# Kernel optimization log

Hardware: AMD Instinct MI355X
Metric: run time of the kernel (lower is better)

The kernel has to match this reference:

```python
import jax, jax.numpy as jnp
import numpy as np

WS = (7, 7, 7)  # window size (h, w, d)
N = WS[0] * WS[1] * WS[2]  # 343
DIM = 192
H = 6
B = 512
NW = 64  # number of distinct window masks; B % NW == 0


def _make_rel_table():
    ch = np.arange(-(WS[0] - 1), WS[0], dtype=np.float32)
    cw = np.arange(-(WS[1] - 1), WS[1], dtype=np.float32)
    cd = np.arange(-(WS[2] - 1), WS[2], dtype=np.float32)
    tbl = np.stack(np.meshgrid(ch, cw, cd, indexing='ij'), axis=-1)[None]  # [1,13,13,13,3]
    tbl[..., 0] /= WS[0] - 1
    tbl[..., 1] /= WS[1] - 1
    tbl[..., 2] /= WS[2] - 1
    tbl *= 8
    tbl = np.sign(tbl) * np.log2(np.abs(tbl) + 1.0) / np.log2(8)
    return tbl.astype(np.float32)


def _make_rp_index():
    coords = np.stack(np.meshgrid(np.arange(WS[0]), np.arange(WS[1]), np.arange(WS[2]), indexing='ij'))
    cf = coords.reshape(3, -1)  # [3, N]
    rel = cf[:, :, None] - cf[:, None, :]  # [3, N, N]
    rel = rel.transpose(1, 2, 0).copy()
    rel[..., 0] += WS[0] - 1
    rel[..., 1] += WS[1] - 1
    rel[..., 2] += WS[2] - 1
    rel[..., 0] *= (2 * WS[1] - 1) * (2 * WS[2] - 1)
    rel[..., 1] *= 2 * WS[2] - 1
    return rel.sum(-1).astype(np.int32)  # [N, N]


def setup_inputs() -> dict:
    key = jax.random.key(0)
    ks = jax.random.split(key, 10)
    s = 0.02
    return {
        'x': jax.random.normal(ks[0], (B, N, DIM), jnp.float32),
        'y': jax.random.normal(ks[1], (B, N, DIM), jnp.float32),
        'mask': jnp.where(jax.random.uniform(ks[2], (NW, N, N)) > 0.5, 0.0, -100.0).astype(jnp.float32),
        'qkv1_w': jax.random.normal(ks[3], (3 * DIM, DIM), jnp.float32) * s,
        'qkv2_w': jax.random.normal(ks[4], (3 * DIM, DIM), jnp.float32) * s,
        'q1_bias': jnp.zeros((DIM,), jnp.float32),
        'v1_bias': jnp.zeros((DIM,), jnp.float32),
        'q2_bias': jnp.zeros((DIM,), jnp.float32),
        'v2_bias': jnp.zeros((DIM,), jnp.float32),
        'logit_scale': jnp.log(10.0 * jnp.ones((H, 1, 1), jnp.float32)),
        'cpb_w1': jax.random.normal(ks[5], (512, 3), jnp.float32) * s,
        'cpb_b1': jnp.zeros((512,), jnp.float32),
        'cpb_w2': jax.random.normal(ks[6], (H, 512), jnp.float32) * s,
        'proj_w': jax.random.normal(ks[7], (DIM, DIM), jnp.float32) * s,
        'proj_b': jnp.zeros((DIM,), jnp.float32),
        'rel_table': jnp.asarray(_make_rel_table()),
        'rp_index': jnp.asarray(_make_rp_index()),
    }


def reference(x, y, mask, qkv1_w, qkv2_w, q1_bias, v1_bias, q2_bias, v2_bias,
              logit_scale, cpb_w1, cpb_b1, cpb_w2, proj_w, proj_b, rel_table, rp_index):
    B_, N_, C = x.shape
    hd = C // H
    qkv1_b = jnp.concatenate([q1_bias, jnp.zeros_like(v1_bias), v1_bias])
    qkv2_b = jnp.concatenate([q2_bias, jnp.zeros_like(v2_bias), v2_bias])
    # [B, N, 3C] -> [3, B, H, N, hd]
    qkv1 = (x @ qkv1_w.T + qkv1_b).reshape(B_, N_, 3, H, hd).transpose(2, 0, 3, 1, 4)
    qkv2 = (y @ qkv2_w.T + qkv2_b).reshape(B_, N_, 3, H, hd).transpose(2, 0, 3, 1, 4)
    q, k, v = qkv2[0], qkv1[1], qkv1[2]
    # cosine attention
    qn = q / jnp.linalg.norm(q, axis=-1, keepdims=True).clip(1e-12)
    kn = k / jnp.linalg.norm(k, axis=-1, keepdims=True).clip(1e-12)
    attn = jnp.einsum('bhnd,bhmd->bhnm', qn, kn)
    scale = jnp.exp(jnp.minimum(logit_scale, jnp.log(jnp.float32(100.0))))
    attn = attn * scale[None]  # [B,H,N,N]
    # continuous position bias
    hbias = jax.nn.relu(rel_table @ cpb_w1.T + cpb_b1) @ cpb_w2.T  # [1,13,13,13,H]
    bias_table = hbias.reshape(-1, H)  # [2197, H]
    rpb = bias_table[rp_index.reshape(-1)].reshape(N_, N_, H).transpose(2, 0, 1)  # [H,N,N]
    rpb = 16.0 * jax.nn.sigmoid(rpb)
    attn = attn + rpb[None]
    # shifted-window mask
    nW = mask.shape[0]
    attn = attn.reshape(B_ // nW, nW, H, N_, N_) + mask[None, :, None]
    attn = attn.reshape(B_, H, N_, N_)
    attn = jax.nn.softmax(attn, axis=-1)
    cross = jnp.einsum('bhnm,bhmd->bnhd', attn, v).reshape(B_, N_, C)
    return cross @ proj_w.T + proj_b
```

## Files before the change

kernel.cpp:

```cpp
#include <hip/hip_runtime.h>

#define HH   6
#define NN   343
#define BB   512
#define DIMC 192
#define MM   (BB*NN)

#define OFF_TABLE 0
#define OFF_R     70400
#define OFF_MB    2968064
#define OFF_QB    4372992
#define OFF_KB    (OFF_QB + 67436544)
#define OFF_VB    (OFF_KB + 67436544)
#define OFF_CROSS (OFF_VB + 67436544)
#define OFF_WB    (OFF_CROSS + 67436544)

typedef __bf16 bf16x8 __attribute__((ext_vector_type(8)));
typedef float  f32x4  __attribute__((ext_vector_type(4)));
typedef float  f32x16 __attribute__((ext_vector_type(16)));

__device__ __forceinline__ f32x4 mfma16(bf16x8 a, bf16x8 b, f32x4 c) {
    return __builtin_amdgcn_mfma_f32_16x16x32_bf16(a, b, c, 0, 0, 0);
}
__device__ __forceinline__ f32x16 mfma32(bf16x8 a, bf16x8 b, f32x16 c) {
    return __builtin_amdgcn_mfma_f32_32x32x16_bf16(a, b, c, 0, 0, 0);
}

__device__ __forceinline__ unsigned pack2(float a, float b) {
    union { __bf16 h[2]; unsigned u; } x;
    x.h[0] = (__bf16)a; x.h[1] = (__bf16)b;
    return x.u;
}
__device__ __forceinline__ void pl32_swap(unsigned &a, unsigned &b) {
    asm volatile("v_permlane32_swap_b32 %0, %1" : "+v"(a), "+v"(b));
}

__global__ __launch_bounds__(256) void cpb_table_kernel(
    const float* __restrict__ rel_table, const float* __restrict__ w1,
    const float* __restrict__ b1, const float* __restrict__ w2,
    float* __restrict__ table)
{
    int i = blockIdx.x;
    int t = threadIdx.x;
    float t0 = rel_table[i*3+0], t1 = rel_table[i*3+1], t2 = rel_table[i*3+2];
    float acc[HH];
    #pragma unroll
    for (int h = 0; h < HH; h++) acc[h] = 0.f;
    for (int j = t; j < 512; j += 256) {
        float hv = w1[j*3+0]*t0 + w1[j*3+1]*t1 + w1[j*3+2]*t2 + b1[j];
        hv = fmaxf(hv, 0.f);
        #pragma unroll
        for (int h = 0; h < HH; h++) acc[h] += w2[h*512+j] * hv;
    }
    __shared__ float red[256*HH];
    #pragma unroll
    for (int h = 0; h < HH; h++) red[t*HH+h] = acc[h];
    __syncthreads();
    for (int s = 128; s > 0; s >>= 1) {
        if (t < s) {
            #pragma unroll
            for (int h = 0; h < HH; h++) red[t*HH+h] += red[(t+s)*HH+h];
        }
        __syncthreads();
    }
    if (t < HH) table[(size_t)i*8 + t] = red[t];
}

__global__ __launch_bounds__(256) void r_kernel(
    const float* __restrict__ table, const int* __restrict__ rp_index,
    float* __restrict__ R)
{
    int id = blockIdx.x*256 + threadIdx.x;
    if (id >= HH*NN*352) return;
    int h   = id / (NN*352);
    int rem = id - h*(NN*352);
    int n   = rem / 352;
    int mc  = rem - n*352;
    float out = 0.f;
    if (mc < NN) {
        float v = table[(size_t)rp_index[n*NN+mc]*8 + h];
        float r = 16.f / (1.f + __expf(-v));
        out = __expf(r - 26.f);
    }
    R[id] = out;
}

__global__ __launch_bounds__(256) void mbits2_kernel(
    const float* __restrict__ mask, unsigned* __restrict__ mb)
{
    int id = blockIdx.x*256 + threadIdx.x;
    if (id >= 64*NN*2) return;
    int hi  = id & 1;
    int row = id >> 1;
    const float* mrow = mask + (size_t)row*NN;
    unsigned* out = mb + (size_t)row*16 + hi*8;
    #pragma unroll
    for (int wd = 0; wd < 6; wd++) {
        unsigned u = 0;
        #pragma unroll
        for (int p = 0; p < 32; p++) {
            int g = 32*wd + p;
            int ks = g >> 4, r = g & 15;
            int m = 32*ks + (r&3) + 8*(r>>2) + 4*hi;
            if (m < NN && mrow[m] > -50.f) u |= (1u << p);
        }
        out[wd] = u;
    }
    out[6] = 0u; out[7] = 0u;
}

__global__ __launch_bounds__(256) void wcvt_kernel(
    const float* __restrict__ qkv1, const float* __restrict__ qkv2,
    const float* __restrict__ proj, __bf16* __restrict__ out)
{
    int i = blockIdx.x*256 + threadIdx.x;
    const int n1 = 110592/4, n2 = 221184/4, n3 = 258048/4;
    if (i >= n3) return;
    const float* src; int off;
    if (i < n1)      { src = qkv1; off = i; }
    else if (i < n2) { src = qkv2; off = i - n1; }
    else             { src = proj; off = i - n2; }
    float4 v = ((const float4*)src)[off];
    __bf16* d = out + (size_t)i*4;
    d[0] = (__bf16)v.x; d[1] = (__bf16)v.y; d[2] = (__bf16)v.z; d[3] = (__bf16)v.w;
}

__global__ __launch_bounds__(256) void gemm_f32in(
    const float* __restrict__ A, const float* __restrict__ ls,
    const __bf16* __restrict__ W0, const float* __restrict__ bias0, int norm0, __bf16* __restrict__ D0,
    const __bf16* __restrict__ W1, const float* __restrict__ bias1, int norm1, __bf16* __restrict__ D1)
{
    __shared__ __bf16 Ws[192*40];
    int m0 = blockIdx.x * 64;
    int t  = threadIdx.x;
    int wave = t >> 6, lane = t & 63, lr = lane & 15, lg = lane >> 4;
    int r = m0 + 16*wave + lr;

    bf16x8 afr[6];
    #pragma unroll
    for (int ks = 0; ks < 6; ks++) {
        const float* ap = A + (size_t)r*DIMC + 32*ks + 8*lg;
        float4 v0 = *(const float4*)ap;
        float4 v1 = *(const float4*)(ap + 4);
        bf16x8 f;
        f[0]=(__bf16)v0.x; f[1]=(__bf16)v0.y; f[2]=(__bf16)v0.z; f[3]=(__bf16)v0.w;
        f[4]=(__bf16)v1.x; f[5]=(__bf16)v1.y; f[6]=(__bf16)v1.z; f[7]=(__bf16)v1.w;
        afr[ks] = f;
    }

    #pragma unroll 1
    for (int phase = 0; phase < 2; phase++) {
        const __bf16* W    = phase ? W1 : W0;
        if (!W) break;
        const float* bias  = phase ? bias1 : bias0;
        int          nrm   = phase ? norm1 : norm0;
        __bf16*      D     = phase ? D1 : D0;
        f32x4 acc[12];
        #pragma unroll
        for (int i = 0; i < 12; i++) acc[i] = (f32x4){0.f,0.f,0.f,0.f};
        for (int ks = 0; ks < 6; ks++) {
            __syncthreads();
            #pragma unroll
            for (int i = 0; i < 3; i++) {
                int c = t + 256*i;
                int row = c >> 2, cg = c & 3;
                uint4 v = *(const uint4*)(W + (size_t)row*DIMC + 32*ks + 8*cg);
                *(uint4*)&Ws[row*40 + 8*cg] = v;
            }
            __syncthreads();
            #pragma unroll
            for (int ct = 0; ct < 12; ct++) {
                bf16x8 bfrag = *(const bf16x8*)&Ws[(16*ct + lr)*40 + 8*lg];
                acc[ct] = mfma16(afr[ks], bfrag, acc[ct]);
            }
        }
        if (bias) {
            #pragma unroll
            for (int ct = 0; ct < 12; ct++) {
                float bv = bias[16*ct + lr];
                #pragma unroll
                for (int reg = 0; reg < 4; reg++) acc[ct][reg] += bv;
            }
        }
        if (nrm) {
            #pragma unroll
            for (int h = 0; h < HH; h++) {
                float sc = 1.f;
                if (nrm == 2) sc = __expf(fminf(ls[h], 4.6051702f)) * 1.4426950408889634f;
                #pragma unroll
                for (int reg = 0; reg < 4; reg++) {
                    float ss = acc[2*h][reg]*acc[2*h][reg] + acc[2*h+1][reg]*acc[2*h+1][reg];
                    ss += __shfl_xor(ss, 1); ss += __shfl_xor(ss, 2);
                    ss += __shfl_xor(ss, 4); ss += __shfl_xor(ss, 8);
                    float f = sc / fmaxf(sqrtf(ss), 1e-12f);
                    acc[2*h][reg]   *= f;
                    acc[2*h+1][reg] *= f;
                }
            }
        }
        #pragma unroll
        for (int ct = 0; ct < 12; ct++) {
            int c = 16*ct + lr;
            #pragma unroll
            for (int reg = 0; reg < 4; reg++) {
                int row = m0 + 16*wave + 4*lg + reg;
                D[(size_t)row*DIMC + c] = (__bf16)acc[ct][reg];
            }
        }
    }
}

__global__ __launch_bounds__(256) void gemm_proj(
    const __bf16* __restrict__ A, const __bf16* __restrict__ W,
    const float* __restrict__ bias, float* __restrict__ D)
{
    __shared__ __bf16 Ws[192*40];
    int m0 = blockIdx.x * 64;
    int t  = threadIdx.x;
    int wave = t >> 6, lane = t & 63, lr = lane & 15, lg = lane >> 4;
    int r = m0 + 16*wave + lr;

    bf16x8 afr[6];
    #pragma unroll
    for (int ks = 0; ks < 6; ks++)
        afr[ks] = *(const bf16x8*)(A + (size_t)r*DIMC + 32*ks + 8*lg);

    f32x4 acc[12];
    #pragma unroll
    for (int i = 0; i < 12; i++) acc[i] = (f32x4){0.f,0.f,0.f,0.f};
    for (int ks = 0; ks < 6; ks++) {
        __syncthreads();
        #pragma unroll
        for (int i = 0; i < 3; i++) {
            int c = t + 256*i;
            int row = c >> 2, cg = c & 3;
            uint4 v = *(const uint4*)(W + (size_t)row*DIMC + 32*ks + 8*cg);
            *(uint4*)&Ws[row*40 + 8*cg] = v;
        }
        __syncthreads();
        #pragma unroll
        for (int ct = 0; ct < 12; ct++) {
            bf16x8 bfrag = *(const bf16x8*)&Ws[(16*ct + lr)*40 + 8*lg];
            acc[ct] = mfma16(afr[ks], bfrag, acc[ct]);
        }
    }
    #pragma unroll
    for (int ct = 0; ct < 12; ct++) {
        int c = 16*ct + lr;
        float bv = bias[c];
        #pragma unroll
        for (int reg = 0; reg < 4; reg++) {
            int row = m0 + 16*wave + 4*lg + reg;
            D[(size_t)row*DIMC + c] = acc[ct][reg] + bv;
        }
    }
}

#define VT_PITCH 360
__global__ __launch_bounds__(256, 4) void attn_kernel(
    const __bf16* __restrict__ qb, const __bf16* __restrict__ kb, const __bf16* __restrict__ vb,
    const float* __restrict__ R, const unsigned* __restrict__ mbits,
    __bf16* __restrict__ cross)
{
    __shared__ __bf16 VTs[32*VT_PITCH];

    int bid = blockIdx.x;
    int bh  = (bid & 7) * (BB*HH/8) + (bid >> 3);
    int b  = bh / HH;
    int h  = bh - b*HH;
    int w  = b & 63;
    int t  = threadIdx.x;

    const __bf16* Kb = kb + ((size_t)b*NN)*DIMC + 32*h;
    const __bf16* Vb = vb + ((size_t)b*NN)*DIMC + 32*h;
    const __bf16* Qb = qb + ((size_t)b*NN)*DIMC + 32*h;

    for (int idx = t; idx < NN*4; idx += 256) {
        int part = idx / NN;
        int m    = idx - part*NN;
        union { uint4 u; __bf16 e[8]; } vv;
        vv.u = *(const uint4*)(Vb + (size_t)m*DIMC + 8*part);
        #pragma unroll
        for (int j = 0; j < 8; j++) VTs[(8*part + j)*VT_PITCH + m] = vv.e[j];
    }
    for (int idx = t; idx < 32*9; idx += 256) {
        int d = idx / 9, m = NN + (idx - d*9);
        VTs[d*VT_PITCH + m] = (__bf16)0.f;
    }
    __syncthreads();

    int wave = t >> 6, lane = t & 63;
    int l31 = lane & 31, hi = lane >> 5;
    const f32x16 zero16 = {0.f,0.f,0.f,0.f,0.f,0.f,0.f,0.f,0.f,0.f,0.f,0.f,0.f,0.f,0.f,0.f};
    const __bf16* VTl = VTs + (size_t)l31*VT_PITCH;

    for (int p = wave; p < 11; p += 4) {
        int q0 = 32*p;
        int rq = min(q0 + l31, NN-1);
        bf16x8 qf0 = *(const bf16x8*)(Qb + (size_t)rq*DIMC + 8*hi);
        bf16x8 qf1 = *(const bf16x8*)(Qb + (size_t)rq*DIMC + 16 + 8*hi);
        const float* Rrow = R + ((size_t)h*NN + rq)*352 + 4*hi;
        const unsigned* mp = mbits + ((size_t)(w*NN + rq))*16 + hi*8;
        uint4 mw = *(const uint4*)mp;
        uint2 mx = *(const uint2*)(mp + 4);
        unsigned long long ma = mw.x | ((unsigned long long)mw.y << 32);
        unsigned long long mbq = mw.z | ((unsigned long long)mw.w << 32);
        unsigned long long mc = mx.x | ((unsigned long long)mx.y << 32);

        f32x16 O = zero16;
        float dsum = 0.f;

        bf16x8 kf0 = *(const bf16x8*)(Kb + (size_t)l31*DIMC + 8*hi);
        bf16x8 kf1 = *(const bf16x8*)(Kb + (size_t)l31*DIMC + 16 + 8*hi);

        for (int ks = 0; ks < 11; ks++) {
            f32x4 rA = *(const f32x4*)(Rrow + 32*ks);
            f32x4 rB = *(const f32x4*)(Rrow + 32*ks + 8);
            f32x4 rC = *(const f32x4*)(Rrow + 32*ks + 16);
            f32x4 rD = *(const f32x4*)(Rrow + 32*ks + 24);
            bf16x8 kf0n = kf0, kf1n = kf1;
            if (ks < 10) {
                int krn = min(32*(ks+1) + l31, NN-1);
                kf0n = *(const bf16x8*)(Kb + (size_t)krn*DIMC + 8*hi);
                kf1n = *(const bf16x8*)(Kb + (size_t)krn*DIMC + 16 + 8*hi);
            }

            f32x16 s = mfma32(kf0, qf0, zero16);
            s = mfma32(kf1, qf1, s);

            unsigned bits = (unsigned)(ma & 0xFFFFu);
            ma = (ma >> 16) | (mbq << 48); mbq = (mbq >> 16) | (mc << 48); mc >>= 16;

            float pv[16];
            #pragma unroll
            for (int r = 0; r < 4; r++) {
                pv[r]    = (bits & (1u << r))      ? __builtin_amdgcn_exp2f(s[r])    * rA[r] : 0.f;
                pv[4+r]  = (bits & (1u << (4+r)))  ? __builtin_amdgcn_exp2f(s[4+r])  * rB[r] : 0.f;
                pv[8+r]  = (bits & (1u << (8+r)))  ? __builtin_amdgcn_exp2f(s[8+r])  * rC[r] : 0.f;
                pv[12+r] = (bits & (1u << (12+r))) ? __builtin_amdgcn_exp2f(s[12+r]) * rD[r] : 0.f;
            }
            {
                float t0 = pv[0]+pv[1], t1 = pv[2]+pv[3], t2 = pv[4]+pv[5], t3 = pv[6]+pv[7];
                float t4 = pv[8]+pv[9], t5 = pv[10]+pv[11], t6 = pv[12]+pv[13], t7 = pv[14]+pv[15];
                dsum += ((t0+t1)+(t2+t3)) + ((t4+t5)+(t6+t7));
            }
            unsigned w0 = pack2(pv[0],  pv[1]),  w1 = pack2(pv[2],  pv[3]);
            unsigned w2 = pack2(pv[4],  pv[5]),  w3 = pack2(pv[6],  pv[7]);
            unsigned w4 = pack2(pv[8],  pv[9]),  w5 = pack2(pv[10], pv[11]);
            unsigned w6 = pack2(pv[12], pv[13]), w7 = pack2(pv[14], pv[15]);
            pl32_swap(w0, w2); pl32_swap(w1, w3);
            pl32_swap(w4, w6); pl32_swap(w5, w7);
            union { unsigned u[4]; bf16x8 f; } fa, fb;
            fa.u[0] = w0; fa.u[1] = w1; fa.u[2] = w2; fa.u[3] = w3;
            fb.u[0] = w4; fb.u[1] = w5; fb.u[2] = w6; fb.u[3] = w7;

            bf16x8 v0 = *(const bf16x8*)&VTl[32*ks + 8*hi];
            bf16x8 v1 = *(const bf16x8*)&VTl[32*ks + 16 + 8*hi];
            O = mfma32(fa.f, v0, O);
            O = mfma32(fb.f, v1, O);

            kf0 = kf0n; kf1 = kf1n;
        }

        dsum += __shfl_xor(dsum, 32);
        float dinv = 1.f / dsum;

        #pragma unroll
        for (int r = 0; r < 16; r++) {
            int off = (r & 3) + 8*(r >> 2) + 4*hi;
            float dv = __shfl(dinv, off);
            int qr = q0 + off;
            if (qr < NN)
                cross[((size_t)b*NN + qr)*DIMC + 32*h + l31] = (__bf16)(O[r] * dv);
        }
    }
}

extern "C" void kernel_launch(void* const* d_in, const int* in_sizes, int n_in,
                              void* d_out, int out_size, void* d_ws, size_t ws_size,
                              hipStream_t stream) {
    const float* x           = (const float*)d_in[0];
    const float* y           = (const float*)d_in[1];
    const float* mask        = (const float*)d_in[2];
    const float* qkv1_w      = (const float*)d_in[3];
    const float* qkv2_w      = (const float*)d_in[4];
    const float* v1_bias     = (const float*)d_in[6];
    const float* q2_bias     = (const float*)d_in[7];
    const float* logit_scale = (const float*)d_in[9];
    const float* cpb_w1      = (const float*)d_in[10];
    const float* cpb_b1      = (const float*)d_in[11];
    const float* cpb_w2      = (const float*)d_in[12];
    const float* proj_w      = (const float*)d_in[13];
    const float* proj_b      = (const float*)d_in[14];
    const float* rel_table   = (const float*)d_in[15];
    const int*   rp_index    = (const int*)d_in[16];

    char* ws = (char*)d_ws;
    float*    table  = (float*)(ws + OFF_TABLE);
    float*    R      = (float*)(ws + OFF_R);
    unsigned* mb     = (unsigned*)(ws + OFF_MB);
    __bf16*   q_bf   = (__bf16*)(ws + OFF_QB);
    __bf16*   k_bf   = (__bf16*)(ws + OFF_KB);
    __bf16*   v_bf   = (__bf16*)(ws + OFF_VB);
    __bf16*   crossb = (__bf16*)(ws + OFF_CROSS);
    __bf16*   wbf    = (__bf16*)(ws + OFF_WB);

    __bf16* w_k    = wbf + 192*DIMC;
    __bf16* w_v    = wbf + 384*DIMC;
    __bf16* w_q    = wbf + 576*DIMC;
    __bf16* w_proj = wbf + 1152*DIMC;

    cpb_table_kernel<<<2197, 256, 0, stream>>>(rel_table, cpb_w1, cpb_b1, cpb_w2, table);
    r_kernel<<<(HH*NN*352 + 255)/256, 256, 0, stream>>>(table, rp_index, R);
    mbits2_kernel<<<(64*NN*2 + 255)/256, 256, 0, stream>>>(mask, mb);
    wcvt_kernel<<<(258048/4 + 255)/256, 256, 0, stream>>>(qkv1_w, qkv2_w, proj_w, wbf);
    gemm_f32in<<<MM/64, 256, 0, stream>>>(x, logit_scale,
                                          w_k, nullptr, 1, k_bf,
                                          w_v, v1_bias, 0, v_bf);
    gemm_f32in<<<MM/64, 256, 0, stream>>>(y, logit_scale,
                                          w_q, q2_bias, 2, q_bf,
                                          nullptr, nullptr, 0, nullptr);

    attn_kernel<<<BB*HH, 256, 0, stream>>>(q_bf, k_bf, v_bf, R, mb, crossb);

    gemm_proj<<<MM/64, 256, 0, stream>>>(crossb, w_proj, proj_b, (float*)d_out);
}
```

Before: 544.1 us.

## Process two query tiles per wave to share K fragment loads

Restructures the attention loop so each wave handles two 32-row query tiles together (tiles wave and wave+4), sharing the K fragment loads and interleaving two independent MFMA/softmax chains. The three leftover tiles are handled afterwards by waves 0-2 on the original single-tile path. The softmax/PV body is factored into a helper. Launch bounds drop from 4 to 3 blocks per SM to leave room for the extra registers, which lowers occupancy. The final tile pass runs on only 3 of 4 waves, so the load is slightly unbalanced.

```diff
diff --git a/kernel.cpp b/kernel.cpp
--- a/kernel.cpp
+++ b/kernel.cpp
@@ -257,7 +257,39 @@
 }
 
 #define VT_PITCH 360
-__global__ __launch_bounds__(256, 4) void attn_kernel(
+__device__ __forceinline__ void soft_pv(
+    const f32x16& s, const f32x4& rA, const f32x4& rB, const f32x4& rC, const f32x4& rD,
+    unsigned bits, float& dsum, f32x16& O, const __bf16* VTl, int ks, int hi)
+{
+    float pv[16];
+    #pragma unroll
+    for (int r = 0; r < 4; r++) {
+        pv[r]    = (bits & (1u << r))      ? __builtin_amdgcn_exp2f(s[r])    * rA[r] : 0.f;
+        pv[4+r]  = (bits & (1u << (4+r)))  ? __builtin_amdgcn_exp2f(s[4+r])  * rB[r] : 0.f;
+        pv[8+r]  = (bits & (1u << (8+r)))  ? __builtin_amdgcn_exp2f(s[8+r])  * rC[r] : 0.f;
+        pv[12+r] = (bits & (1u << (12+r))) ? __builtin_amdgcn_exp2f(s[12+r]) * rD[r] : 0.f;
+    }
+    {
+        float t0 = pv[0]+pv[1], t1 = pv[2]+pv[3], t2 = pv[4]+pv[5], t3 = pv[6]+pv[7];
+        float t4 = pv[8]+pv[9], t5 = pv[10]+pv[11], t6 = pv[12]+pv[13], t7 = pv[14]+pv[15];
+        dsum += ((t0+t1)+(t2+t3)) + ((t4+t5)+(t6+t7));
+    }
+    unsigned w0 = pack2(pv[0],  pv[1]),  w1 = pack2(pv[2],  pv[3]);
+    unsigned w2 = pack2(pv[4],  pv[5]),  w3 = pack2(pv[6],  pv[7]);
+    unsigned w4 = pack2(pv[8],  pv[9]),  w5 = pack2(pv[10], pv[11]);
+    unsigned w6 = pack2(pv[12], pv[13]), w7 = pack2(pv[14], pv[15]);
+    pl32_swap(w0, w2); pl32_swap(w1, w3);
+    pl32_swap(w4, w6); pl32_swap(w5, w7);
+    union { unsigned u[4]; bf16x8 f; } fa, fb;
+    fa.u[0] = w0; fa.u[1] = w1; fa.u[2] = w2; fa.u[3] = w3;
+    fb.u[0] = w4; fb.u[1] = w5; fb.u[2] = w6; fb.u[3] = w7;
+    bf16x8 v0 = *(const bf16x8*)&VTl[32*ks + 8*hi];
+    bf16x8 v1 = *(const bf16x8*)&VTl[32*ks + 16 + 8*hi];
+    O = mfma32(fa.f, v0, O);
+    O = mfma32(fb.f, v1, O);
+}
+
+__global__ __launch_bounds__(256, 3) void attn_kernel(
     const __bf16* __restrict__ qb, const __bf16* __restrict__ kb, const __bf16* __restrict__ vb,
     const float* __restrict__ R, const unsigned* __restrict__ mbits,
     __bf16* __restrict__ cross)
@@ -294,8 +326,81 @@
     const f32x16 zero16 = {0.f,0.f,0.f,0.f,0.f,0.f,0.f,0.f,0.f,0.f,0.f,0.f,0.f,0.f,0.f,0.f};
     const __bf16* VTl = VTs + (size_t)l31*VT_PITCH;
 
-    for (int p = wave; p < 11; p += 4) {
-        int q0 = 32*p;
+    {
+        int q00 = 32*wave, q01 = 32*(wave+4);
+        int rq0 = q00 + l31, rq1 = q01 + l31;
+        bf16x8 qa0 = *(const bf16x8*)(Qb + (size_t)rq0*DIMC + 8*hi);
+        bf16x8 qa1 = *(const bf16x8*)(Qb + (size_t)rq0*DIMC + 16 + 8*hi);
+        bf16x8 qc0 = *(const bf16x8*)(Qb + (size_t)rq1*DIMC + 8*hi);
+        bf16x8 qc1 = *(const bf16x8*)(Qb + (size_t)rq1*DIMC + 16 + 8*hi);
+        const float* Rrow0 = R + ((size_t)h*NN + rq0)*352 + 4*hi;
+        const float* Rrow1 = R + ((size_t)h*NN + rq1)*352 + 4*hi;
+        const unsigned* mp0 = mbits + ((size_t)(w*NN + rq0))*16 + hi*8;
+        const unsigned* mp1 = mbits + ((size_t)(w*NN + rq1))*16 + hi*8;
+        uint4 mw0 = *(const uint4*)mp0;  uint2 mx0 = *(const uint2*)(mp0 + 4);
+        uint4 mw1 = *(const uint4*)mp1;  uint2 mx1 = *(const uint2*)(mp1 + 4);
+        unsigned long long ma0 = mw0.x | ((unsigned long long)mw0.y << 32);
+        unsigned long long mb0 = mw0.z | ((unsigned long long)mw0.w << 32);
+        unsigned long long mc0 = mx0.x | ((unsigned long long)mx0.y << 32);
+        unsigned long long ma1 = mw1.x | ((unsigned long long)mw1.y << 32);
+        unsigned long long mb1 = mw1.z | ((unsigned long long)mw1.w << 32);
+        unsigned long long mc1 = mx1.x | ((unsigned long long)mx1.y << 32);
+
+        f32x16 O0 = zero16, O1 = zero16;
+        float dsum0 = 0.f, dsum1 = 0.f;
+
+        bf16x8 kf0 = *(const bf16x8*)(Kb + (size_t)l31*DIMC + 8*hi);
+        bf16x8 kf1 = *(const bf16x8*)(Kb + (size_t)l31*DIMC + 16 + 8*hi);
+
+        for (int ks = 0; ks < 11; ks++) {
+            f32x4 rA0 = *(const f32x4*)(Rrow0 + 32*ks);
+            f32x4 rB0 = *(const f32x4*)(Rrow0 + 32*ks + 8);
+            f32x4 rC0 = *(const f32x4*)(Rrow0 + 32*ks + 16);
+            f32x4 rD0 = *(const f32x4*)(Rrow0 + 32*ks + 24);
+            f32x4 rA1 = *(const f32x4*)(Rrow1 + 32*ks);
+            f32x4 rB1 = *(const f32x4*)(Rrow1 + 32*ks + 8);
+            f32x4 rC1 = *(const f32x4*)(Rrow1 + 32*ks + 16);
+            f32x4 rD1 = *(const f32x4*)(Rrow1 + 32*ks + 24);
+            bf16x8 kf0n = kf0, kf1n = kf1;
+            if (ks < 10) {
+                int krn = min(32*(ks+1) + l31, NN-1);
+                kf0n = *(const bf16x8*)(Kb + (size_t)krn*DIMC + 8*hi);
+                kf1n = *(const bf16x8*)(Kb + (size_t)krn*DIMC + 16 + 8*hi);
+            }
+
+            f32x16 s0 = mfma32(kf0, qa0, zero16);
+            s0 = mfma32(kf1, qa1, s0);
+            f32x16 s1 = mfma32(kf0, qc0, zero16);
+            s1 = mfma32(kf1, qc1, s1);
+
+            unsigned bits0 = (unsigned)(ma0 & 0xFFFFu);
+            ma0 = (ma0 >> 16) | (mb0 << 48); mb0 = (mb0 >> 16) | (mc0 << 48); mc0 >>= 16;
+            unsigned bits1 = (unsigned)(ma1 & 0xFFFFu);
+            ma1 = (ma1 >> 16) | (mb1 << 48); mb1 = (mb1 >> 16) | (mc1 << 48); mc1 >>= 16;
+
+            soft_pv(s0, rA0, rB0, rC0, rD0, bits0, dsum0, O0, VTl, ks, hi);
+            soft_pv(s1, rA1, rB1, rC1, rD1, bits1, dsum1, O1, VTl, ks, hi);
+
+            kf0 = kf0n; kf1 = kf1n;
+        }
+
+        dsum0 += __shfl_xor(dsum0, 32);
+        dsum1 += __shfl_xor(dsum1, 32);
+        float dinv0 = 1.f / dsum0;
+        float dinv1 = 1.f / dsum1;
+
+        #pragma unroll
+        for (int r = 0; r < 16; r++) {
+            int off = (r & 3) + 8*(r >> 2) + 4*hi;
+            float dv0 = __shfl(dinv0, off);
+            float dv1 = __shfl(dinv1, off);
+            cross[((size_t)b*NN + q00 + off)*DIMC + 32*h + l31] = (__bf16)(O0[r] * dv0);
+            cross[((size_t)b*NN + q01 + off)*DIMC + 32*h + l31] = (__bf16)(O1[r] * dv1);
+        }
+    }
+
+    if (wave < 3) {
+        int q0 = 32*(8 + wave);
         int rq = min(q0 + l31, NN-1);
         bf16x8 qf0 = *(const bf16x8*)(Qb + (size_t)rq*DIMC + 8*hi);
         bf16x8 qf1 = *(const bf16x8*)(Qb + (size_t)rq*DIMC + 16 + 8*hi);
@@ -331,33 +436,7 @@
             unsigned bits = (unsigned)(ma & 0xFFFFu);
             ma = (ma >> 16) | (mbq << 48); mbq = (mbq >> 16) | (mc << 48); mc >>= 16;
 
-            float pv[16];
-            #pragma unroll
-            for (int r = 0; r < 4; r++) {
-                pv[r]    = (bits & (1u << r))      ? __builtin_amdgcn_exp2f(s[r])    * rA[r] : 0.f;
-                pv[4+r]  = (bits & (1u << (4+r)))  ? __builtin_amdgcn_exp2f(s[4+r])  * rB[r] : 0.f;
-                pv[8+r]  = (bits & (1u << (8+r)))  ? __builtin_amdgcn_exp2f(s[8+r])  * rC[r] : 0.f;
-                pv[12+r] = (bits & (1u << (12+r))) ? __builtin_amdgcn_exp2f(s[12+r]) * rD[r] : 0.f;
-            }
-            {
-                float t0 = pv[0]+pv[1], t1 = pv[2]+pv[3], t2 = pv[4]+pv[5], t3 = pv[6]+pv[7];
-                float t4 = pv[8]+pv[9], t5 = pv[10]+pv[11], t6 = pv[12]+pv[13], t7 = pv[14]+pv[15];
-                dsum += ((t0+t1)+(t2+t3)) + ((t4+t5)+(t6+t7));
-            }
-            unsigned w0 = pack2(pv[0],  pv[1]),  w1 = pack2(pv[2],  pv[3]);
-            unsigned w2 = pack2(pv[4],  pv[5]),  w3 = pack2(pv[6],  pv[7]);
-            unsigned w4 = pack2(pv[8],  pv[9]),  w5 = pack2(pv[10], pv[11]);
-            unsigned w6 = pack2(pv[12], pv[13]), w7 = pack2(pv[14], pv[15]);
-            pl32_swap(w0, w2); pl32_swap(w1, w3);
-            pl32_swap(w4, w6); pl32_swap(w5, w7);
-            union { unsigned u[4]; bf16x8 f; } fa, fb;
-            fa.u[0] = w0; fa.u[1] = w1; fa.u[2] = w2; fa.u[3] = w3;
-            fb.u[0] = w4; fb.u[1] = w5; fb.u[2] = w6; fb.u[3] = w7;
-
-            bf16x8 v0 = *(const bf16x8*)&VTl[32*ks + 8*hi];
-            bf16x8 v1 = *(const bf16x8*)&VTl[32*ks + 16 + 8*hi];
-            O = mfma32(fa.f, v0, O);
-            O = mfma32(fb.f, v1, O);
+            soft_pv(s, rA, rB, rC, rD, bits, dsum, O, VTl, ks, hi);
 
             kf0 = kf0n; kf1 = kf1n;
         }
```

New measurement: 543.7 us. No clear change (-0.1%).
